# Optimization experiments

Hardware: AMD Instinct MI355X
Metric: run time of the kernel (lower is better)

The kernel has to match this reference:

```python
import jax, jax.numpy as jnp
import numpy as np

B = 65536
D = 512
R = 64  # min(64, D) reflections (cap_householder_refl=True)


def setup_inputs() -> dict:
    key = jax.random.key(0)
    k1, k2 = jax.random.split(key)
    x = jax.random.normal(k1, (B, D), dtype=jnp.float32)
    sldj = jnp.zeros((B,), dtype=jnp.float32)
    householder_params = jax.random.normal(k2, (D, R), dtype=jnp.float32)
    return {"x": x, "sldj": sldj, "householder_params": householder_params}


def reference(x, sldj, householder_params):
    # Sequential Householder reflections: x <- x - 2 (x . u_hat) u_hat
    # params: (D, R); unconditioned, so u is shared across the batch.
    us = householder_params.T  # (R, D), scanned in forward order i = 0..R-1

    def step(xc, u):
        unit_u = u / jnp.linalg.norm(u)          # (D,)
        scalar = xc @ unit_u                      # (B,)
        xc = xc - 2.0 * scalar[:, None] * unit_u  # rank-1 update
        return xc, None

    out, _ = jax.lax.scan(step, x, us)
    return out, sldj
```

## Files before the change

kernel.cpp:

```cpp
#include <hip/hip_runtime.h>

typedef __attribute__((ext_vector_type(8))) short bf16x8;
typedef __attribute__((ext_vector_type(4))) float f32x4;
typedef __attribute__((ext_vector_type(4))) unsigned int u32x4;

#define DD 512
#define RR 64
#define BTOT 65536
#define BM 128
#define BN 128
#define BKT 64
#define NKT (DD / BKT)

static __device__ __forceinline__ unsigned short f2bf(float f) {
    union { float f; unsigned u; } v; v.f = f;
    unsigned r = v.u + 0x7fffu + ((v.u >> 16) & 1u);
    return (unsigned short)(r >> 16);
}

static __device__ __forceinline__ unsigned pack2bf(float x, float y) {
    union { float f; unsigned u; } a, b;
    a.f = x; b.f = y;
    unsigned ax = a.u + 0x8000u, bx = b.u + 0x8000u;
    return __builtin_amdgcn_perm(bx, ax, 0x07060302u);
}

__global__ void normalize_kernel(const float* __restrict__ P, float* __restrict__ U) {
    int i = blockIdx.x;
    int t = threadIdx.x;
    __shared__ float red[4];
    float a = P[t * RR + i];
    float b = P[(t + 256) * RR + i];
    float p = a * a + b * b;
#pragma unroll
    for (int off = 32; off > 0; off >>= 1) p += __shfl_down(p, off);
    if ((t & 63) == 0) red[t >> 6] = p;
    __syncthreads();
    float s = red[0] + red[1] + red[2] + red[3];
    float inv = 1.0f / sqrtf(s);
    U[i * DD + t]       = a * inv;
    U[i * DD + t + 256] = b * inv;
}

__global__ void compose_kernel(const float* __restrict__ U,
                               unsigned short* __restrict__ Mt,
                               const float* __restrict__ sldj,
                               float* __restrict__ sldj_out) {
    int c = blockIdx.x;
    int l = threadIdx.x;

    ((float2*)sldj_out)[(size_t)c * 64 + l] = ((const float2*)sldj)[(size_t)c * 64 + l];

    float v[8], u[8], un[8];
#pragma unroll
    for (int j = 0; j < 8; ++j) v[j] = (64 * j + l == c) ? 1.0f : 0.0f;
#pragma unroll
    for (int j = 0; j < 8; ++j) u[j] = U[64 * j + l];

    for (int i = 0; i < RR; ++i) {
        int inext = (i + 1 < RR) ? i + 1 : i;
#pragma unroll
        for (int j = 0; j < 8; ++j) un[j] = U[inext * DD + 64 * j + l];
        float s0 = v[0] * u[0] + v[1] * u[1];
        float s1 = v[2] * u[2] + v[3] * u[3];
        float s2 = v[4] * u[4] + v[5] * u[5];
        float s3 = v[6] * u[6] + v[7] * u[7];
        float s = (s0 + s1) + (s2 + s3);
#pragma unroll
        for (int off = 32; off > 0; off >>= 1) s += __shfl_xor(s, off);
        s *= 2.0f;
#pragma unroll
        for (int j = 0; j < 8; ++j) v[j] -= s * u[j];
#pragma unroll
        for (int j = 0; j < 8; ++j) u[j] = un[j];
    }
#pragma unroll
    for (int j = 0; j < 8; ++j) Mt[(size_t)(64 * j + l) * DD + c] = f2bf(v[j]);
}

__launch_bounds__(256, 3)
__global__ void gemm_kernel(const float* __restrict__ X,
                            const unsigned short* __restrict__ Mt,
                            float* __restrict__ out) {
    __shared__ __attribute__((aligned(16))) unsigned short lA[BM * BKT];
    __shared__ __attribute__((aligned(16))) unsigned short lB[BN * BKT];

    int t = threadIdx.x;
    int bid = blockIdx.x;

    int row_t = (bid >> 5) * 8 + (bid & 7);
    int col_t = (bid >> 3) & 3;
    int row0 = row_t * BM;
    int col0 = col_t * BN;

    int wave = t >> 6, lane = t & 63;
    int wm = wave >> 1, wn = wave & 1;
    int quad = lane >> 4, l16 = lane & 15;

    int arow = t >> 1, ah = t & 1;
    const float4* aSrc = (const float4*)(X + (size_t)(row0 + arow) * DD + ah * 32);
    unsigned short* aDst0 = lA + arow * 64;
    int s_base = 4 * ah;
    int arx = arow & 7;

    int bln = lane >> 3;
    int bg = (lane & 7) ^ bln;
    const unsigned short* bSrc = Mt + (size_t)(col0 + wave * 32 + bln) * DD + bg * 8;

    const unsigned short* aRd = lA + (wm * 64 + l16) * 64;
    const unsigned short* bRd = lB + (wn * 64 + l16) * 64;
    int so0 = (quad ^ (l16 & 7)) * 8;
    int so1 = ((4 + quad) ^ (l16 & 7)) * 8;

    f32x4 acc[4][4] = {};

    float4 av[8];
#pragma unroll
    for (int j = 0; j < 8; ++j) av[j] = aSrc[j];

#pragma unroll 1
    for (int kt = 0; kt < NKT; ++kt) {
#pragma unroll
        for (int j4 = 0; j4 < 4; ++j4) {
            u32x4 wv;
            float4 x0 = av[2 * j4], x1 = av[2 * j4 + 1];
            wv.x = pack2bf(x0.x, x0.y);
            wv.y = pack2bf(x0.z, x0.w);
            wv.z = pack2bf(x1.x, x1.y);
            wv.w = pack2bf(x1.z, x1.w);
            *(u32x4*)(aDst0 + ((s_base + j4) ^ arx) * 8) = wv;
        }
#pragma unroll
        for (int q = 0; q < 4; ++q) {
            __builtin_amdgcn_global_load_lds(
                (const __attribute__((address_space(1))) unsigned int*)(bSrc + (size_t)q * 8 * DD + kt * BKT),
                (__attribute__((address_space(3))) unsigned int*)(lB + (wave * 4 + q) * 512),
                16, 0, 0);
        }
        __builtin_amdgcn_sched_barrier(0);
        if (kt + 1 < NKT) {
            const float4* apn = aSrc + (kt + 1) * (BKT / 4);
#pragma unroll
            for (int j = 0; j < 8; ++j) av[j] = apn[j];
            asm volatile("s_waitcnt vmcnt(8) lgkmcnt(0)" ::: "memory");
        } else {
            asm volatile("s_waitcnt vmcnt(0) lgkmcnt(0)" ::: "memory");
        }
        __builtin_amdgcn_s_barrier();
        asm volatile("" ::: "memory");

#pragma unroll
        for (int sl = 0; sl < 2; ++sl) {
            int so = sl ? so1 : so0;
            bf16x8 af[4], bf[4];
#pragma unroll
            for (int mt = 0; mt < 4; ++mt) af[mt] = *(const bf16x8*)(aRd + mt * 1024 + so);
#pragma unroll
            for (int nt = 0; nt < 4; ++nt) bf[nt] = *(const bf16x8*)(bRd + nt * 1024 + so);
#pragma unroll
            for (int mt = 0; mt < 4; ++mt)
#pragma unroll
                for (int nt = 0; nt < 4; ++nt)
                    acc[mt][nt] = __builtin_amdgcn_mfma_f32_16x16x32_bf16(af[mt], bf[nt], acc[mt][nt], 0, 0, 0);
        }
        asm volatile("s_waitcnt lgkmcnt(0)" ::: "memory");
        __builtin_amdgcn_s_barrier();
        asm volatile("" ::: "memory");
    }

#pragma unroll
    for (int mt = 0; mt < 4; ++mt) {
#pragma unroll
        for (int r = 0; r < 4; ++r) {
            int row = row0 + wm * 64 + mt * 16 + quad * 4 + r;
            float* orow = out + (size_t)row * DD + col0 + wn * 64 + l16;
#pragma unroll
            for (int nt = 0; nt < 4; ++nt)
                orow[nt * 16] = acc[mt][nt][r];
        }
    }
}

extern "C" void kernel_launch(void* const* d_in, const int* in_sizes, int n_in,
                              void* d_out, int out_size, void* d_ws, size_t ws_size,
                              hipStream_t stream) {
    const float* x      = (const float*)d_in[0];
    const float* sldj   = (const float*)d_in[1];
    const float* params = (const float*)d_in[2];
    float* out = (float*)d_out;

    float* U = (float*)d_ws;
    unsigned short* Mt = (unsigned short*)((char*)d_ws + RR * DD * sizeof(float));

    normalize_kernel<<<RR, 256, 0, stream>>>(params, U);
    compose_kernel<<<DD, 64, 0, stream>>>(U, Mt, sldj, out + (size_t)BTOT * DD);
    gemm_kernel<<<(BTOT / BM) * (DD / BN), 256, 0, stream>>>(x, Mt, out);
}
```

Baseline: 300.4 us.

## Double-buffer GEMM LDS tiles with smaller K-tile and higher occupancy

Halves the K tile to 32 and double-buffers both A and B shared-memory tiles, so the next tile's bf16 conversion, store and async global-to-LDS load overlap the current tile's MFMAs. Each iteration now needs only one barrier instead of two. Launch bounds rise to 4 blocks per CU, since total LDS per block stays the same. The cost is twice as many loop iterations, each with less MFMA work to hide latency, and tighter register limits from the higher occupancy target.

```diff
diff --git a/kernel.cpp b/kernel.cpp
--- a/kernel.cpp
+++ b/kernel.cpp
@@ -9,8 +9,8 @@
 #define BTOT 65536
 #define BM 128
 #define BN 128
-#define BKT 64
-#define NKT (DD / BKT)
+#define BK 32
+#define NKT (DD / BK)
 
 static __device__ __forceinline__ unsigned short f2bf(float f) {
     union { float f; unsigned u; } v; v.f = f;
@@ -78,12 +78,12 @@
     for (int j = 0; j < 8; ++j) Mt[(size_t)(64 * j + l) * DD + c] = f2bf(v[j]);
 }
 
-__launch_bounds__(256, 3)
+__launch_bounds__(256, 4)
 __global__ void gemm_kernel(const float* __restrict__ X,
                             const unsigned short* __restrict__ Mt,
                             float* __restrict__ out) {
-    __shared__ __attribute__((aligned(16))) unsigned short lA[BM * BKT];
-    __shared__ __attribute__((aligned(16))) unsigned short lB[BN * BKT];
+    __shared__ __attribute__((aligned(16))) unsigned short lA2[2][BM * BK];
+    __shared__ __attribute__((aligned(16))) unsigned short lB2[2][BN * BK];
 
     int t = threadIdx.x;
     int bid = blockIdx.x;
@@ -97,75 +97,114 @@
     int wm = wave >> 1, wn = wave & 1;
     int quad = lane >> 4, l16 = lane & 15;
 
-    int arow = t >> 1, ah = t & 1;
-    const float4* aSrc = (const float4*)(X + (size_t)(row0 + arow) * DD + ah * 32);
-    unsigned short* aDst0 = lA + arow * 64;
-    int s_base = 4 * ah;
-    int arx = arow & 7;
-
-    int bln = lane >> 3;
-    int bg = (lane & 7) ^ bln;
-    const unsigned short* bSrc = Mt + (size_t)(col0 + wave * 32 + bln) * DD + bg * 8;
-
-    const unsigned short* aRd = lA + (wm * 64 + l16) * 64;
-    const unsigned short* bRd = lB + (wn * 64 + l16) * 64;
-    int so0 = (quad ^ (l16 & 7)) * 8;
-    int so1 = ((4 + quad) ^ (l16 & 7)) * 8;
+    int ar = t >> 1, ah = t & 1;
+    const float4* aSrcT = (const float4*)(X + (size_t)(row0 + ar) * DD) + ah * 4;
+    int arx = ar & 3;
+    int as0 = ((2 * ah) ^ arx) * 8;
+    int as1 = ((2 * ah + 1) ^ arx) * 8;
+    int aDstRow = ar * BK;
+
+    int bg = (lane & 3) ^ ((lane >> 2) & 3);
+    const unsigned short* bSrc = Mt + (size_t)(col0 + wave * 32 + (lane >> 2)) * DD + bg * 8;
+    int bDst = wave * 2 * 512;
+
+    int fro = (quad ^ (l16 & 3)) * 8;
+    int aRdRow = (wm * 64 + l16) * BK + fro;
+    int bRdRow = (wn * 64 + l16) * BK + fro;
+
+    unsigned short* lA = &lA2[0][0];
+    unsigned short* lB = &lB2[0][0];
 
     f32x4 acc[4][4] = {};
-
-    float4 av[8];
-#pragma unroll
-    for (int j = 0; j < 8; ++j) av[j] = aSrc[j];
-
+    float4 av[4];
+
+#pragma unroll
+    for (int j = 0; j < 4; ++j) av[j] = aSrcT[j];
+#pragma unroll
+    for (int q = 0; q < 2; ++q)
+        __builtin_amdgcn_global_load_lds(
+            (const __attribute__((address_space(1))) unsigned int*)(bSrc + (size_t)q * 16 * DD),
+            (__attribute__((address_space(3))) unsigned int*)(lB + bDst + q * 512),
+            16, 0, 0);
+    __builtin_amdgcn_sched_barrier(0);
+    {
+        u32x4 w0, w1;
+        w0.x = pack2bf(av[0].x, av[0].y); w0.y = pack2bf(av[0].z, av[0].w);
+        w0.z = pack2bf(av[1].x, av[1].y); w0.w = pack2bf(av[1].z, av[1].w);
+        w1.x = pack2bf(av[2].x, av[2].y); w1.y = pack2bf(av[2].z, av[2].w);
+        w1.z = pack2bf(av[3].x, av[3].y); w1.w = pack2bf(av[3].z, av[3].w);
+        *(u32x4*)(lA + aDstRow + as0) = w0;
+        *(u32x4*)(lA + aDstRow + as1) = w1;
+    }
+    __builtin_amdgcn_sched_barrier(0);
+#pragma unroll
+    for (int j = 0; j < 4; ++j) av[j] = aSrcT[8 + j];
+    __builtin_amdgcn_sched_barrier(0);
+    asm volatile("s_waitcnt vmcnt(4) lgkmcnt(0)" ::: "memory");
+    __builtin_amdgcn_s_barrier();
+    asm volatile("" ::: "memory");
+
+    int p = 0;
 #pragma unroll 1
-    for (int kt = 0; kt < NKT; ++kt) {
-#pragma unroll
-        for (int j4 = 0; j4 < 4; ++j4) {
-            u32x4 wv;
-            float4 x0 = av[2 * j4], x1 = av[2 * j4 + 1];
-            wv.x = pack2bf(x0.x, x0.y);
-            wv.y = pack2bf(x0.z, x0.w);
-            wv.z = pack2bf(x1.x, x1.y);
-            wv.w = pack2bf(x1.z, x1.w);
-            *(u32x4*)(aDst0 + ((s_base + j4) ^ arx) * 8) = wv;
-        }
-#pragma unroll
-        for (int q = 0; q < 4; ++q) {
+    for (int kt = 0; kt < NKT - 1; ++kt) {
+        unsigned short* lAs = lA + (p ^ 1) * (BM * BK);
+        unsigned short* lBs = lB + (p ^ 1) * (BN * BK);
+        {
+            u32x4 w0, w1;
+            w0.x = pack2bf(av[0].x, av[0].y); w0.y = pack2bf(av[0].z, av[0].w);
+            w0.z = pack2bf(av[1].x, av[1].y); w0.w = pack2bf(av[1].z, av[1].w);
+            w1.x = pack2bf(av[2].x, av[2].y); w1.y = pack2bf(av[2].z, av[2].w);
+            w1.z = pack2bf(av[3].x, av[3].y); w1.w = pack2bf(av[3].z, av[3].w);
+            *(u32x4*)(lAs + aDstRow + as0) = w0;
+            *(u32x4*)(lAs + aDstRow + as1) = w1;
+        }
+#pragma unroll
+        for (int q = 0; q < 2; ++q)
             __builtin_amdgcn_global_load_lds(
-                (const __attribute__((address_space(1))) unsigned int*)(bSrc + (size_t)q * 8 * DD + kt * BKT),
-                (__attribute__((address_space(3))) unsigned int*)(lB + (wave * 4 + q) * 512),
+                (const __attribute__((address_space(1))) unsigned int*)(bSrc + (size_t)q * 16 * DD + (kt + 1) * BK),
+                (__attribute__((address_space(3))) unsigned int*)(lBs + bDst + q * 512),
                 16, 0, 0);
-        }
         __builtin_amdgcn_sched_barrier(0);
-        if (kt + 1 < NKT) {
-            const float4* apn = aSrc + (kt + 1) * (BKT / 4);
-#pragma unroll
-            for (int j = 0; j < 8; ++j) av[j] = apn[j];
-            asm volatile("s_waitcnt vmcnt(8) lgkmcnt(0)" ::: "memory");
-        } else {
+        if (kt < NKT - 2) {
+#pragma unroll
+            for (int j = 0; j < 4; ++j) av[j] = aSrcT[(kt + 2) * 8 + j];
+        }
+        __builtin_amdgcn_sched_barrier(0);
+        {
+            const unsigned short* lAc = lA + p * (BM * BK);
+            const unsigned short* lBc = lB + p * (BN * BK);
+            bf16x8 af[4], bf[4];
+#pragma unroll
+            for (int mt = 0; mt < 4; ++mt) af[mt] = *(const bf16x8*)(lAc + aRdRow + mt * 512);
+#pragma unroll
+            for (int nt = 0; nt < 4; ++nt) bf[nt] = *(const bf16x8*)(lBc + bRdRow + nt * 512);
+#pragma unroll
+            for (int mt = 0; mt < 4; ++mt)
+#pragma unroll
+                for (int nt = 0; nt < 4; ++nt)
+                    acc[mt][nt] = __builtin_amdgcn_mfma_f32_16x16x32_bf16(af[mt], bf[nt], acc[mt][nt], 0, 0, 0);
+        }
+        if (kt < NKT - 2)
+            asm volatile("s_waitcnt vmcnt(4) lgkmcnt(0)" ::: "memory");
+        else
             asm volatile("s_waitcnt vmcnt(0) lgkmcnt(0)" ::: "memory");
-        }
         __builtin_amdgcn_s_barrier();
         asm volatile("" ::: "memory");
-
-#pragma unroll
-        for (int sl = 0; sl < 2; ++sl) {
-            int so = sl ? so1 : so0;
-            bf16x8 af[4], bf[4];
-#pragma unroll
-            for (int mt = 0; mt < 4; ++mt) af[mt] = *(const bf16x8*)(aRd + mt * 1024 + so);
-#pragma unroll
-            for (int nt = 0; nt < 4; ++nt) bf[nt] = *(const bf16x8*)(bRd + nt * 1024 + so);
-#pragma unroll
-            for (int mt = 0; mt < 4; ++mt)
-#pragma unroll
-                for (int nt = 0; nt < 4; ++nt)
-                    acc[mt][nt] = __builtin_amdgcn_mfma_f32_16x16x32_bf16(af[mt], bf[nt], acc[mt][nt], 0, 0, 0);
-        }
-        asm volatile("s_waitcnt lgkmcnt(0)" ::: "memory");
-        __builtin_amdgcn_s_barrier();
-        asm volatile("" ::: "memory");
+        p ^= 1;
+    }
+    {
+        const unsigned short* lAc = lA + p * (BM * BK);
+        const unsigned short* lBc = lB + p * (BN * BK);
+        bf16x8 af[4], bf[4];
+#pragma unroll
+        for (int mt = 0; mt < 4; ++mt) af[mt] = *(const bf16x8*)(lAc + aRdRow + mt * 512);
+#pragma unroll
+        for (int nt = 0; nt < 4; ++nt) bf[nt] = *(const bf16x8*)(lBc + bRdRow + nt * 512);
+#pragma unroll
+        for (int mt = 0; mt < 4; ++mt)
+#pragma unroll
+            for (int nt = 0; nt < 4; ++nt)
+                acc[mt][nt] = __builtin_amdgcn_mfma_f32_16x16x32_bf16(af[mt], bf[nt], acc[mt][nt], 0, 0, 0);
     }
 
 #pragma unroll
```

Measured after the change: 287.7 us. 1.04x faster.
